# Kernel optimization log

Hardware: AMD Instinct MI355X
Metric: run time of the kernel (lower is better)

Reference implementation:

```python
import jax, jax.numpy as jnp
import numpy as np

UNITS = 64
NUM_LEVELS = 4
ORDER = 4  # order=-1 defaults to num_levels
NUM_FEATURES = 64  # 63 input features + 1 time channel
LEN_TENSORS = NUM_LEVELS * (NUM_LEVELS + 1) // 2  # 10


def setup_inputs() -> dict:
    key = jax.random.key(0)
    k1, k2 = jax.random.split(key)
    X = jax.random.normal(k1, (32, 2048, 63), dtype=jnp.float32)
    # learned low-rank kernel [num_features, len_tensors, units]; small scale keeps
    # higher-level signature products numerically tame
    kernel = jax.random.normal(k2, (NUM_FEATURES, LEN_TENSORS, UNITS), dtype=jnp.float32) * 0.02
    return {"X": X, "kernel": kernel}


def _ecumsum(x):
    # exclusive cumulative sum along time axis (axis=1), forward direction
    return jnp.cumsum(x, axis=1) - x


def reference(X, kernel):
    B, T, _ = X.shape
    # add_time=True: linear time channel in [-1, 1]
    t = jnp.arange(T, dtype=X.dtype) * (2.0 / (T - 1.0)) - 1.0
    time = jnp.broadcast_to(t[None, :, None], (B, T, 1))
    Xa = jnp.concatenate([time, X], axis=-1)  # [B, T, F]
    # low-rank projection: [B, T, len_tensors, units]
    M = jnp.einsum('btf,fku->btku', Xa, kernel)
    # difference=True: forward increments, zero-padded at t=0
    M = jnp.concatenate([jnp.zeros_like(M[:, :1]), M[:, 1:] - M[:, :-1]], axis=1)

    # level 1
    out = jnp.sum(M[..., 0, :], axis=1)  # [B, units]

    k = 1
    for m in range(1, NUM_LEVELS):
        R = [M[..., k, :]]  # list of [B, T, units]
        k += 1
        for i in range(1, m + 1):
            d = min(i + 1, ORDER)
            A = sum(R)
            Mk = M[..., k, :]
            R_next = [Mk * _ecumsum(A)]
            for j in range(1, d):
                R_next.append(Mk * R[j - 1] / jnp.asarray(j + 1, dtype=X.dtype))
            k += 1
            R = R_next
        out = out + jnp.sum(sum(R), axis=1)
    return out
```

## Files before the change

kernel.cpp:

```cpp
#include <hip/hip_runtime.h>


#define TT 2048
#define NFX 63
#define KT 10
#define NU 64
#define NQ 17
#define NCC 32
#define NSEG 4

#define MAPS_BYTES (32u * NCC * NQ * NU * 4u)
#define KWB_BYTES  (2u * 40960u * 2u)
#define PLANE      40960u

typedef __attribute__((ext_vector_type(16))) float f32x16v;
typedef __attribute__((ext_vector_type(8)))  short bf16x8v;

enum {Qo=0, Qa1, Qa3, QaA, Qa6, QaP, QaQ, Qd1, Qd3, QdA, Qd6, QdP, QdQ,
      QtA3, QtP6, QtQP, QtQ6};

__device__ __forceinline__ unsigned short bf16_rne(float x) {
  unsigned int u = __float_as_uint(x);
  unsigned int r = (u + 0x7FFFu + ((u >> 16) & 1u)) >> 16;
  return (unsigned short)r;
}
__device__ __forceinline__ float bf16f(unsigned short h) {
  return __uint_as_float(((unsigned int)h) << 16);
}

__device__ __forceinline__ void compose_maps(const float* q1, const float* q2,
                                             float* r)
{
  r[Qo]  = q1[Qo] + q2[Qo]
         + q2[Qa1]*q1[Qd1] + q2[Qa3]*q1[Qd3] + q2[QaA]*q1[QdA]
         + q2[Qa6]*q1[Qd6] + q2[QaP]*q1[QdP] + q2[QaQ]*q1[QdQ];
  r[Qa1] = q1[Qa1] + q2[Qa1];
  r[Qa3] = q1[Qa3] + q2[Qa3] + q1[QtA3]*q2[QaA];
  r[QaA] = q1[QaA] + q2[QaA];
  r[Qa6] = q1[Qa6] + q2[Qa6] + q1[QtP6]*q2[QaP] + q1[QtQ6]*q2[QaQ];
  r[QaP] = q1[QaP] + q2[QaP] + q1[QtQP]*q2[QaQ];
  r[QaQ] = q1[QaQ] + q2[QaQ];
  r[Qd1] = q1[Qd1] + q2[Qd1];
  r[Qd3] = q1[Qd3] + q2[Qd3];
  r[QdA] = q1[QdA] + q2[QdA] + q2[QtA3]*q1[Qd3];
  r[Qd6] = q1[Qd6] + q2[Qd6];
  r[QdP] = q1[QdP] + q2[QdP] + q2[QtP6]*q1[Qd6];
  r[QdQ] = q1[QdQ] + q2[QdQ] + q2[QtQP]*q1[QdP] + q2[QtQ6]*q1[Qd6];
  r[QtA3] = q1[QtA3] + q2[QtA3];
  r[QtP6] = q1[QtP6] + q2[QtP6];
  r[QtQP] = q1[QtQP] + q2[QtQP];
  r[QtQ6] = q1[QtQ6] + q2[QtQ6] + q2[QtQP]*q1[QtP6];
}

__global__ __launch_bounds__(256)
void lrsig_prep_kernel(const float* __restrict__ Kw,
                       unsigned short* __restrict__ kwb)
{
  int e = blockIdx.x * 256 + threadIdx.x;
  int j  = e & 7;
  int l  = (e >> 3) & 63;
  int ks = (e >> 9) & 3;
  int ub = (e >> 11) & 1;
  int nt = e >> 12;
  int f = ks * 16 + (l >> 5) * 8 + j;
  int u = ub * 32 + (l & 31);
  float x = Kw[(f * KT + nt) * NU + u];
  unsigned short hi = bf16_rne(x);
  unsigned short lo = bf16_rne(x - bf16f(hi));
  kwb[e] = hi;
  kwb[PLANE + e] = lo;
}

template<int KBASE, int NNT>
__device__ __forceinline__ void mfma_phase_pf(
    const unsigned short* __restrict__ kwb,
    const bf16x8v (&ah)[4], const bf16x8v (&al)[4],
    int l, int ub, f32x16v (&acc)[NNT])
{
#pragma unroll
  for (int t = 0; t < NNT; ++t)
#pragma unroll
    for (int i = 0; i < 16; ++i) acc[t][i] = 0.f;

  bf16x8v bh[2][4], bl[2][4];
#pragma unroll
  for (int ks = 0; ks < 4; ++ks) {
    const unsigned short* bp =
        kwb + (((KBASE * 2 + ub) * 4 + ks) * 512) + l * 8;
    bh[0][ks] = *(const bf16x8v*)(bp);
    bl[0][ks] = *(const bf16x8v*)(bp + PLANE);
  }
#pragma unroll
  for (int t = 0; t < NNT; ++t) {
    if (t + 1 < NNT) {
#pragma unroll
      for (int ks = 0; ks < 4; ++ks) {
        const unsigned short* bp =
            kwb + ((((KBASE + t + 1) * 2 + ub) * 4 + ks) * 512) + l * 8;
        bh[(t + 1) & 1][ks] = *(const bf16x8v*)(bp);
        bl[(t + 1) & 1][ks] = *(const bf16x8v*)(bp + PLANE);
      }
    }
#pragma unroll
    for (int ks = 0; ks < 4; ++ks) {
      acc[t] = __builtin_amdgcn_mfma_f32_32x32x16_bf16(ah[ks], bh[t & 1][ks], acc[t], 0, 0, 0);
      acc[t] = __builtin_amdgcn_mfma_f32_32x32x16_bf16(al[ks], bh[t & 1][ks], acc[t], 0, 0, 0);
      acc[t] = __builtin_amdgcn_mfma_f32_32x32x16_bf16(ah[ks], bl[t & 1][ks], acc[t], 0, 0, 0);
    }
  }
}

__global__ __launch_bounds__(256)
void lrsig_chunk_kernel(const float* __restrict__ X,
                        const unsigned short* __restrict__ kwb,
                        float* __restrict__ wmaps)
{
  __shared__ __align__(16) float smemf[8192];
  char* smem = (char*)smemf;
  float* rawf = smemf + 4096;

  const int b   = blockIdx.y;
  const int c   = blockIdx.x;
  const int tid = threadIdx.x;
  const int l   = tid & 63;
  const int w   = tid >> 6;
  const int rt  = w >> 1;
  const int ub  = w & 1;
  const int col = l & 31;
  const int hi8 = l >> 5;
  const int t0  = c * 64;

  float sv[16];
  {
    const float* Xb = X + (size_t)b * TT * NFX;
    const int base = (t0 - 1) * NFX;
#pragma unroll
    for (int ii = 0; ii < 16; ++ii) {
      int i = tid + ii * 256;
      int off = base + i + ((c == 0 && i < NFX) ? NFX : 0);
      sv[ii] = (i < 65 * NFX) ? Xb[off] : 0.f;
    }
  }

  bf16x8v bhA[3][4], blA[3][4];
#pragma unroll
  for (int t = 0; t < 3; ++t)
#pragma unroll
    for (int ks = 0; ks < 4; ++ks) {
      const unsigned short* bp = kwb + (((t * 2 + ub) * 4 + ks) * 512) + l * 8;
      bhA[t][ks] = *(const bf16x8v*)(bp);
      blA[t][ks] = *(const bf16x8v*)(bp + PLANE);
    }

#pragma unroll
  for (int ii = 0; ii < 16; ++ii) {
    int i = tid + ii * 256;
    if (i < 65 * NFX) rawf[i] = sv[ii];
  }
  __syncthreads();

  {
    float v0[16], v1[16];
#pragma unroll
    for (int ii = 0; ii < 16; ++ii) {
      int e = tid + ii * 256;
      if (e < 64 * NFX) { v0[ii] = rawf[e]; v1[ii] = rawf[e + NFX]; }
    }
#pragma unroll
    for (int ii = 0; ii < 16; ++ii) {
      int e = tid + ii * 256;
      if (e < 64 * NFX) {
        int r2 = e / NFX;
        int c2 = e - r2 * NFX;
        float d = v1[ii] - v0[ii];
        unsigned short h  = bf16_rne(d);
        unsigned short lo = bf16_rne(d - bf16f(h));
        int byte = r2 * 128 + ((2 * (c2 + 1)) ^ ((r2 & 7) << 4));
        *(unsigned short*)(smem + byte)        = h;
        *(unsigned short*)(smem + 8192 + byte) = lo;
      }
    }
  }
  if (tid < 64) {
    int r2 = tid;
    float d = (t0 + r2 == 0) ? 0.f : (2.0f / 2047.0f);
    unsigned short h  = bf16_rne(d);
    unsigned short lo = bf16_rne(d - bf16f(h));
    int byte = r2 * 128 + ((0) ^ ((r2 & 7) << 4));
    *(unsigned short*)(smem + byte)        = h;
    *(unsigned short*)(smem + 8192 + byte) = lo;
  }
  __syncthreads();

  const int row = rt * 32 + col;
  const int colbase = ub * 32 + col;

  bf16x8v ah[4], al[4];
#pragma unroll
  for (int ks = 0; ks < 4; ++ks) {
    const int f0 = ks * 16 + hi8 * 8;
    const int abyte = row * 128 + ((2 * f0) ^ ((row & 7) << 4));
    ah[ks] = *(const bf16x8v*)(smem + abyte);
    al[ks] = *(const bf16x8v*)(smem + 8192 + abyte);
  }

  float Ao[4], Aa1[4], Ad1[4];
  {
    f32x16v acc[3];
#pragma unroll
    for (int t = 0; t < 3; ++t)
#pragma unroll
      for (int i = 0; i < 16; ++i) acc[t][i] = 0.f;
#pragma unroll
    for (int ks = 0; ks < 4; ++ks)
#pragma unroll
      for (int t = 0; t < 3; ++t) {
        acc[t] = __builtin_amdgcn_mfma_f32_32x32x16_bf16(ah[ks], bhA[t][ks], acc[t], 0, 0, 0);
        acc[t] = __builtin_amdgcn_mfma_f32_32x32x16_bf16(al[ks], bhA[t][ks], acc[t], 0, 0, 0);
        acc[t] = __builtin_amdgcn_mfma_f32_32x32x16_bf16(ah[ks], blA[t][ks], acc[t], 0, 0, 0);
      }
#pragma unroll
    for (int j = 0; j < 4; ++j) {
      float o = 0.f, a1 = 0.f, lc1 = 0.f;
#pragma unroll
      for (int i = 0; i < 4; ++i) {
        const int r = 4 * j + i;
        float m0 = acc[0][r], m1 = acc[1][r], m2 = acc[2][r];
        o   += m0 + m2 * (lc1 + 0.5f * m1);
        a1  += m2;
        lc1 += m1;
      }
      Ao[j] = o; Aa1[j] = a1; Ad1[j] = lc1;
    }
  }

  float Ba3[4], BaA[4], Bd3[4], BdA[4], BtA3[4];
  {
    f32x16v acc[3];
    mfma_phase_pf<3, 3>(kwb, ah, al, l, ub, acc);
#pragma unroll
    for (int j = 0; j < 4; ++j) {
      float o = 0.f, a3 = 0.f, aA = 0.f, lc3 = 0.f, lcA = 0.f, g4 = 0.f;
#pragma unroll
      for (int i = 0; i < 4; ++i) {
        const int r = 4 * j + i;
        float m3 = acc[0][r], m4 = acc[1][r], m5 = acc[2][r];
        float s0 = m4 * lc3;
        float s1 = 0.5f * m4 * m3;
        o   += m5 * (lcA + 0.5f * s0 + (1.f/3.f) * s1);
        a3  += m5 * (g4 + 0.5f * m4);
        aA  += m5;
        lcA += s0 + s1;
        g4  += m4;
        lc3 += m3;
      }
      Ao[j] += o;
      Ba3[j] = a3; BaA[j] = aA; Bd3[j] = lc3; BdA[j] = lcA; BtA3[j] = g4;
    }
  }

  float tot[NQ];
  {
    f32x16v acc[4];
    mfma_phase_pf<6, 4>(kwb, ah, al, l, ub, acc);
#pragma unroll
    for (int j = 0; j < 4; ++j) {
      float o = 0.f, a6 = 0.f, aP = 0.f, aQ = 0.f;
      float lc6 = 0.f, lcP = 0.f, lcQ = 0.f, g7 = 0.f, g8 = 0.f, hh = 0.f;
#pragma unroll
      for (int i = 0; i < 4; ++i) {
        const int r = 4 * j + i;
        float m6 = acc[0][r], m7 = acc[1][r], m8 = acc[2][r], m9 = acc[3][r];
        float p0 = m7 * lc6;
        float p1 = 0.5f * m7 * m6;
        float q0 = m8 * lcP;
        float q1 = 0.5f * m8 * p0;
        float q2 = (1.f/3.f) * m8 * p1;
        o   += m9 * (lcQ + 0.5f * q0 + (1.f/3.f) * q1 + 0.25f * q2);
        a6  += m9 * (hh + m8 * (0.5f * g7 + (1.f/6.f) * m7));
        aP  += m9 * (g8 + 0.5f * m8);
        aQ  += m9;
        hh  += m8 * (g7 + 0.5f * m7);
        lcP += p0 + p1;
        lcQ += q0 + q1 + q2;
        g7 += m7; g8 += m8; lc6 += m6;
      }
      float mj[NQ];
      mj[Qo] = Ao[j] + o;
      mj[Qa1] = Aa1[j]; mj[Qa3] = Ba3[j]; mj[QaA] = BaA[j];
      mj[Qa6] = a6;     mj[QaP] = aP;     mj[QaQ] = aQ;
      mj[Qd1] = Ad1[j]; mj[Qd3] = Bd3[j]; mj[QdA] = BdA[j];
      mj[Qd6] = lc6;    mj[QdP] = lcP;    mj[QdQ] = lcQ;
      mj[QtA3] = BtA3[j]; mj[QtP6] = g7;  mj[QtQP] = g8; mj[QtQ6] = hh;

      float q1v[NQ], q2v[NQ], m8r[NQ];
#pragma unroll
      for (int q = 0; q < NQ; ++q) {
        float oth = __shfl_xor(mj[q], 32);
        q1v[q] = hi8 ? oth : mj[q];
        q2v[q] = hi8 ? mj[q] : oth;
      }
      compose_maps(q1v, q2v, m8r);

      if (j == 0) {
#pragma unroll
        for (int q = 0; q < NQ; ++q) tot[q] = m8r[q];
      } else {
        float nt_[NQ];
        compose_maps(tot, m8r, nt_);
#pragma unroll
        for (int q = 0; q < NQ; ++q) tot[q] = nt_[q];
      }
    }
  }

  if (hi8 == 0) {
    float* p = &rawf[(rt * NQ) * NU + colbase];
#pragma unroll
    for (int q = 0; q < NQ; ++q) p[q * NU] = tot[q];
  }
  __syncthreads();

  if (tid < NU) {
    const int uu = tid;
    float q1v[NQ], q2v[NQ], rv[NQ];
#pragma unroll
    for (int q = 0; q < NQ; ++q) {
      q1v[q] = rawf[(0 * NQ + q) * NU + uu];
      q2v[q] = rawf[(1 * NQ + q) * NU + uu];
    }
    compose_maps(q1v, q2v, rv);
    float* p = &wmaps[(((size_t)b * NCC + c) * NQ) * NU + uu];
#pragma unroll
    for (int q = 0; q < NQ; ++q) p[q * NU] = rv[q];
  }
}

__global__ __launch_bounds__(256)
void lrsig_partial_kernel(const float* __restrict__ wmaps,
                          float* __restrict__ part)
{
  const int b   = blockIdx.x;
  const int seg = threadIdx.x >> 6;
  const int u   = threadIdx.x & 63;
  float tot[NQ];
  {
    const float* p0 = &wmaps[(((size_t)b * NCC + seg * 8) * NQ) * NU + u];
#pragma unroll
    for (int q = 0; q < NQ; ++q) tot[q] = p0[q * NU];
  }
  for (int i = 1; i < 8; ++i) {
    const float* p = &wmaps[(((size_t)b * NCC + seg * 8 + i) * NQ) * NU + u];
    float m[NQ], r[NQ];
#pragma unroll
    for (int q = 0; q < NQ; ++q) m[q] = p[q * NU];
    compose_maps(tot, m, r);
#pragma unroll
    for (int q = 0; q < NQ; ++q) tot[q] = r[q];
  }
  float* d = &part[(((size_t)b * NSEG + seg) * NQ) * NU + u];
#pragma unroll
  for (int q = 0; q < NQ; ++q) d[q * NU] = tot[q];
}

__global__ __launch_bounds__(64)
void lrsig_final_kernel(const float* __restrict__ part,
                        float* __restrict__ out)
{
  const int b = blockIdx.x;
  const int u = threadIdx.x;
  float c1 = 0.f, c3 = 0.f, cA = 0.f, c6 = 0.f, cP = 0.f, cQ = 0.f, o = 0.f;
#pragma unroll
  for (int s = 0; s < NSEG; ++s) {
    const float* p = &part[(((size_t)b * NSEG + s) * NQ) * NU + u];
    float q[NQ];
#pragma unroll
    for (int i = 0; i < NQ; ++i) q[i] = p[i * NU];
    o  += q[0] + q[1]*c1 + q[2]*c3 + q[3]*cA + q[4]*c6 + q[5]*cP + q[6]*cQ;
    cA += q[13]*c3 + q[9];
    cQ += q[15]*cP + q[16]*c6 + q[12];
    cP += q[14]*c6 + q[11];
    c1 += q[7]; c3 += q[8]; c6 += q[10];
  }
  out[b * 64 + u] = o;
}

extern "C" void kernel_launch(void* const* d_in, const int* in_sizes, int n_in,
                              void* d_out, int out_size, void* d_ws, size_t ws_size,
                              hipStream_t stream) {
  const float* X  = (const float*)d_in[0];
  const float* Kw = (const float*)d_in[1];
  float* out = (float*)d_out;
  float* wmaps = (float*)d_ws;
  unsigned short* kwb = (unsigned short*)((char*)d_ws + MAPS_BYTES);
  float* part = (float*)((char*)d_ws + MAPS_BYTES + KWB_BYTES);

  hipLaunchKernelGGL(lrsig_prep_kernel, dim3(160), dim3(256), 0, stream,
                     Kw, kwb);
  hipLaunchKernelGGL(lrsig_chunk_kernel, dim3(NCC, 32), dim3(256), 0, stream,
                     X, kwb, wmaps);
  hipLaunchKernelGGL(lrsig_partial_kernel, dim3(32), dim3(256), 0, stream,
                     wmaps, part);
  hipLaunchKernelGGL(lrsig_final_kernel, dim3(32), dim3(64), 0, stream,
                     part, out);
}
```

Before: 48.35 us.

## Fuse partial and final combine kernels, stream B operands, tree-reduce chunk maps

Merges the partial and final combine kernels into one launch that passes the per-segment maps through shared memory instead of a global scratch buffer. This removes one kernel launch and a global round trip. In the chunk kernel, the B operands for all ten projection tiles are now streamed through one double buffer, replacing the register-resident phase-A preload and the templated helper. The sequential fold of the four 8-row maps becomes a balanced tree of compositions, which shortens the dependency chain but keeps more values live in registers.

After: 48.60 us. No clear change (+0.5%).

```diff
diff --git a/kernel.cpp b/kernel.cpp
--- a/kernel.cpp
+++ b/kernel.cpp
@@ -10,7 +10,6 @@
 #define NSEG 4
 
 #define MAPS_BYTES (32u * NCC * NQ * NU * 4u)
-#define KWB_BYTES  (2u * 40960u * 2u)
 #define PLANE      40960u
 
 typedef __attribute__((ext_vector_type(16))) float f32x16v;
@@ -71,44 +70,24 @@
   kwb[PLANE + e] = lo;
 }
 
-template<int KBASE, int NNT>
-__device__ __forceinline__ void mfma_phase_pf(
-    const unsigned short* __restrict__ kwb,
-    const bf16x8v (&ah)[4], const bf16x8v (&al)[4],
-    int l, int ub, f32x16v (&acc)[NNT])
-{
-#pragma unroll
-  for (int t = 0; t < NNT; ++t)
-#pragma unroll
-    for (int i = 0; i < 16; ++i) acc[t][i] = 0.f;
-
-  bf16x8v bh[2][4], bl[2][4];
-#pragma unroll
-  for (int ks = 0; ks < 4; ++ks) {
-    const unsigned short* bp =
-        kwb + (((KBASE * 2 + ub) * 4 + ks) * 512) + l * 8;
-    bh[0][ks] = *(const bf16x8v*)(bp);
-    bl[0][ks] = *(const bf16x8v*)(bp + PLANE);
-  }
-#pragma unroll
-  for (int t = 0; t < NNT; ++t) {
-    if (t + 1 < NNT) {
-#pragma unroll
-      for (int ks = 0; ks < 4; ++ks) {
-        const unsigned short* bp =
-            kwb + ((((KBASE + t + 1) * 2 + ub) * 4 + ks) * 512) + l * 8;
-        bh[(t + 1) & 1][ks] = *(const bf16x8v*)(bp);
-        bl[(t + 1) & 1][ks] = *(const bf16x8v*)(bp + PLANE);
-      }
-    }
-#pragma unroll
-    for (int ks = 0; ks < 4; ++ks) {
-      acc[t] = __builtin_amdgcn_mfma_f32_32x32x16_bf16(ah[ks], bh[t & 1][ks], acc[t], 0, 0, 0);
-      acc[t] = __builtin_amdgcn_mfma_f32_32x32x16_bf16(al[ks], bh[t & 1][ks], acc[t], 0, 0, 0);
-      acc[t] = __builtin_amdgcn_mfma_f32_32x32x16_bf16(ah[ks], bl[t & 1][ks], acc[t], 0, 0, 0);
-    }
-  }
-}
+#define LOADB(BUF, S) do {                                                   \
+  _Pragma("unroll")                                                          \
+  for (int ks = 0; ks < 4; ++ks) {                                           \
+    const unsigned short* bp = kwb + ((((S) * 2 + ub) * 4 + ks) * 512) + l*8;\
+    bh##BUF[ks] = *(const bf16x8v*)(bp);                                     \
+    bl##BUF[ks] = *(const bf16x8v*)(bp + PLANE);                             \
+  } } while (0)
+
+#define MFMA12(ACC, BUF) do {                                                \
+  _Pragma("unroll")                                                          \
+  for (int ks = 0; ks < 4; ++ks) {                                           \
+    ACC = __builtin_amdgcn_mfma_f32_32x32x16_bf16(ah[ks], bh##BUF[ks], ACC, 0,0,0); \
+    ACC = __builtin_amdgcn_mfma_f32_32x32x16_bf16(al[ks], bh##BUF[ks], ACC, 0,0,0); \
+    ACC = __builtin_amdgcn_mfma_f32_32x32x16_bf16(ah[ks], bl##BUF[ks], ACC, 0,0,0); \
+  } } while (0)
+
+#define ZERO(ACC) do { _Pragma("unroll")                                     \
+  for (int zi = 0; zi < 16; ++zi) ACC[zi] = 0.f; } while (0)
 
 __global__ __launch_bounds__(256)
 void lrsig_chunk_kernel(const float* __restrict__ X,
@@ -142,15 +121,8 @@
     }
   }
 
-  bf16x8v bhA[3][4], blA[3][4];
-#pragma unroll
-  for (int t = 0; t < 3; ++t)
-#pragma unroll
-    for (int ks = 0; ks < 4; ++ks) {
-      const unsigned short* bp = kwb + (((t * 2 + ub) * 4 + ks) * 512) + l * 8;
-      bhA[t][ks] = *(const bf16x8v*)(bp);
-      blA[t][ks] = *(const bf16x8v*)(bp + PLANE);
-    }
+  bf16x8v bh0[4], bl0[4], bh1[4], bl1[4];
+  LOADB(0, 0);
 
 #pragma unroll
   for (int ii = 0; ii < 16; ++ii) {
@@ -205,27 +177,21 @@
   }
 
   float Ao[4], Aa1[4], Ad1[4];
-  {
-    f32x16v acc[3];
-#pragma unroll
-    for (int t = 0; t < 3; ++t)
-#pragma unroll
-      for (int i = 0; i < 16; ++i) acc[t][i] = 0.f;
-#pragma unroll
-    for (int ks = 0; ks < 4; ++ks)
-#pragma unroll
-      for (int t = 0; t < 3; ++t) {
-        acc[t] = __builtin_amdgcn_mfma_f32_32x32x16_bf16(ah[ks], bhA[t][ks], acc[t], 0, 0, 0);
-        acc[t] = __builtin_amdgcn_mfma_f32_32x32x16_bf16(al[ks], bhA[t][ks], acc[t], 0, 0, 0);
-        acc[t] = __builtin_amdgcn_mfma_f32_32x32x16_bf16(ah[ks], blA[t][ks], acc[t], 0, 0, 0);
-      }
+  float Ba3[4], BaA[4], Bd3[4], BdA[4], BtA3[4];
+
+  {
+    f32x16v accA[3];
+    ZERO(accA[0]); ZERO(accA[1]); ZERO(accA[2]);
+    LOADB(1, 1);  MFMA12(accA[0], 0);
+    LOADB(0, 2);  MFMA12(accA[1], 1);
+    LOADB(1, 3);  MFMA12(accA[2], 0);
 #pragma unroll
     for (int j = 0; j < 4; ++j) {
       float o = 0.f, a1 = 0.f, lc1 = 0.f;
 #pragma unroll
       for (int i = 0; i < 4; ++i) {
         const int r = 4 * j + i;
-        float m0 = acc[0][r], m1 = acc[1][r], m2 = acc[2][r];
+        float m0 = accA[0][r], m1 = accA[1][r], m2 = accA[2][r];
         o   += m0 + m2 * (lc1 + 0.5f * m1);
         a1  += m2;
         lc1 += m1;
@@ -234,17 +200,19 @@
     }
   }
 
-  float Ba3[4], BaA[4], Bd3[4], BdA[4], BtA3[4];
-  {
-    f32x16v acc[3];
-    mfma_phase_pf<3, 3>(kwb, ah, al, l, ub, acc);
+  {
+    f32x16v accB[3];
+    ZERO(accB[0]); ZERO(accB[1]); ZERO(accB[2]);
+    LOADB(0, 4);  MFMA12(accB[0], 1);
+    LOADB(1, 5);  MFMA12(accB[1], 0);
+    LOADB(0, 6);  MFMA12(accB[2], 1);
 #pragma unroll
     for (int j = 0; j < 4; ++j) {
       float o = 0.f, a3 = 0.f, aA = 0.f, lc3 = 0.f, lcA = 0.f, g4 = 0.f;
 #pragma unroll
       for (int i = 0; i < 4; ++i) {
         const int r = 4 * j + i;
-        float m3 = acc[0][r], m4 = acc[1][r], m5 = acc[2][r];
+        float m3 = accB[0][r], m4 = accB[1][r], m5 = accB[2][r];
         float s0 = m4 * lc3;
         float s1 = 0.5f * m4 * m3;
         o   += m5 * (lcA + 0.5f * s0 + (1.f/3.f) * s1);
@@ -261,8 +229,14 @@
 
   float tot[NQ];
   {
-    f32x16v acc[4];
-    mfma_phase_pf<6, 4>(kwb, ah, al, l, ub, acc);
+    f32x16v accC[4];
+    ZERO(accC[0]); ZERO(accC[1]); ZERO(accC[2]); ZERO(accC[3]);
+    LOADB(1, 7);  MFMA12(accC[0], 0);
+    LOADB(0, 8);  MFMA12(accC[1], 1);
+    LOADB(1, 9);  MFMA12(accC[2], 0);
+                  MFMA12(accC[3], 1);
+
+    float mjv[4][NQ];
 #pragma unroll
     for (int j = 0; j < 4; ++j) {
       float o = 0.f, a6 = 0.f, aP = 0.f, aQ = 0.f;
@@ -270,7 +244,7 @@
 #pragma unroll
       for (int i = 0; i < 4; ++i) {
         const int r = 4 * j + i;
-        float m6 = acc[0][r], m7 = acc[1][r], m8 = acc[2][r], m9 = acc[3][r];
+        float m6 = accC[0][r], m7 = accC[1][r], m8 = accC[2][r], m9 = accC[3][r];
         float p0 = m7 * lc6;
         float p1 = 0.5f * m7 * m6;
         float q0 = m8 * lcP;
@@ -285,33 +259,31 @@
         lcQ += q0 + q1 + q2;
         g7 += m7; g8 += m8; lc6 += m6;
       }
-      float mj[NQ];
-      mj[Qo] = Ao[j] + o;
-      mj[Qa1] = Aa1[j]; mj[Qa3] = Ba3[j]; mj[QaA] = BaA[j];
-      mj[Qa6] = a6;     mj[QaP] = aP;     mj[QaQ] = aQ;
-      mj[Qd1] = Ad1[j]; mj[Qd3] = Bd3[j]; mj[QdA] = BdA[j];
-      mj[Qd6] = lc6;    mj[QdP] = lcP;    mj[QdQ] = lcQ;
-      mj[QtA3] = BtA3[j]; mj[QtP6] = g7;  mj[QtQP] = g8; mj[QtQ6] = hh;
-
-      float q1v[NQ], q2v[NQ], m8r[NQ];
+      mjv[j][Qo] = Ao[j] + o;
+      mjv[j][Qa1] = Aa1[j]; mjv[j][Qa3] = Ba3[j]; mjv[j][QaA] = BaA[j];
+      mjv[j][Qa6] = a6;     mjv[j][QaP] = aP;     mjv[j][QaQ] = aQ;
+      mjv[j][Qd1] = Ad1[j]; mjv[j][Qd3] = Bd3[j]; mjv[j][QdA] = BdA[j];
+      mjv[j][Qd6] = lc6;    mjv[j][QdP] = lcP;    mjv[j][QdQ] = lcQ;
+      mjv[j][QtA3] = BtA3[j]; mjv[j][QtP6] = g7;
+      mjv[j][QtQP] = g8;      mjv[j][QtQ6] = hh;
+    }
+
+    float m8v[4][NQ];
+#pragma unroll
+    for (int j = 0; j < 4; ++j) {
+      float q1v[NQ], q2v[NQ];
 #pragma unroll
       for (int q = 0; q < NQ; ++q) {
-        float oth = __shfl_xor(mj[q], 32);
-        q1v[q] = hi8 ? oth : mj[q];
-        q2v[q] = hi8 ? mj[q] : oth;
-      }
-      compose_maps(q1v, q2v, m8r);
-
-      if (j == 0) {
-#pragma unroll
-        for (int q = 0; q < NQ; ++q) tot[q] = m8r[q];
-      } else {
-        float nt_[NQ];
-        compose_maps(tot, m8r, nt_);
-#pragma unroll
-        for (int q = 0; q < NQ; ++q) tot[q] = nt_[q];
-      }
-    }
+        float oth = __shfl_xor(mjv[j][q], 32);
+        q1v[q] = hi8 ? oth : mjv[j][q];
+        q2v[q] = hi8 ? mjv[j][q] : oth;
+      }
+      compose_maps(q1v, q2v, m8v[j]);
+    }
+    float m16a[NQ], m16b[NQ];
+    compose_maps(m8v[0], m8v[1], m16a);
+    compose_maps(m8v[2], m8v[3], m16b);
+    compose_maps(m16a, m16b, tot);
   }
 
   if (hi8 == 0) {
@@ -337,12 +309,14 @@
 }
 
 __global__ __launch_bounds__(256)
-void lrsig_partial_kernel(const float* __restrict__ wmaps,
-                          float* __restrict__ part)
+void lrsig_combine_kernel(const float* __restrict__ wmaps,
+                          float* __restrict__ out)
 {
+  __shared__ float sm[NSEG * NQ * NU];
   const int b   = blockIdx.x;
   const int seg = threadIdx.x >> 6;
   const int u   = threadIdx.x & 63;
+
   float tot[NQ];
   {
     const float* p0 = &wmaps[(((size_t)b * NCC + seg * 8) * NQ) * NU + u];
@@ -358,31 +332,26 @@
 #pragma unroll
     for (int q = 0; q < NQ; ++q) tot[q] = r[q];
   }
-  float* d = &part[(((size_t)b * NSEG + seg) * NQ) * NU + u];
-#pragma unroll
-  for (int q = 0; q < NQ; ++q) d[q * NU] = tot[q];
-}
-
-__global__ __launch_bounds__(64)
-void lrsig_final_kernel(const float* __restrict__ part,
-                        float* __restrict__ out)
-{
-  const int b = blockIdx.x;
-  const int u = threadIdx.x;
-  float c1 = 0.f, c3 = 0.f, cA = 0.f, c6 = 0.f, cP = 0.f, cQ = 0.f, o = 0.f;
-#pragma unroll
-  for (int s = 0; s < NSEG; ++s) {
-    const float* p = &part[(((size_t)b * NSEG + s) * NQ) * NU + u];
-    float q[NQ];
-#pragma unroll
-    for (int i = 0; i < NQ; ++i) q[i] = p[i * NU];
-    o  += q[0] + q[1]*c1 + q[2]*c3 + q[3]*cA + q[4]*c6 + q[5]*cP + q[6]*cQ;
-    cA += q[13]*c3 + q[9];
-    cQ += q[15]*cP + q[16]*c6 + q[12];
-    cP += q[14]*c6 + q[11];
-    c1 += q[7]; c3 += q[8]; c6 += q[10];
-  }
-  out[b * 64 + u] = o;
+#pragma unroll
+  for (int q = 0; q < NQ; ++q) sm[(seg * NQ + q) * NU + u] = tot[q];
+  __syncthreads();
+
+  if (threadIdx.x < NU) {
+    const int uu = threadIdx.x;
+    float c1 = 0.f, c3 = 0.f, cA = 0.f, c6 = 0.f, cP = 0.f, cQ = 0.f, o = 0.f;
+#pragma unroll
+    for (int s = 0; s < NSEG; ++s) {
+      float q[NQ];
+#pragma unroll
+      for (int i = 0; i < NQ; ++i) q[i] = sm[(s * NQ + i) * NU + uu];
+      o  += q[0] + q[1]*c1 + q[2]*c3 + q[3]*cA + q[4]*c6 + q[5]*cP + q[6]*cQ;
+      cA += q[13]*c3 + q[9];
+      cQ += q[15]*cP + q[16]*c6 + q[12];
+      cP += q[14]*c6 + q[11];
+      c1 += q[7]; c3 += q[8]; c6 += q[10];
+    }
+    out[b * 64 + uu] = o;
+  }
 }
 
 extern "C" void kernel_launch(void* const* d_in, const int* in_sizes, int n_in,
@@ -393,14 +362,11 @@
   float* out = (float*)d_out;
   float* wmaps = (float*)d_ws;
   unsigned short* kwb = (unsigned short*)((char*)d_ws + MAPS_BYTES);
-  float* part = (float*)((char*)d_ws + MAPS_BYTES + KWB_BYTES);
 
   hipLaunchKernelGGL(lrsig_prep_kernel, dim3(160), dim3(256), 0, stream,
                      Kw, kwb);
   hipLaunchKernelGGL(lrsig_chunk_kernel, dim3(NCC, 32), dim3(256), 0, stream,
                      X, kwb, wmaps);
-  hipLaunchKernelGGL(lrsig_partial_kernel, dim3(32), dim3(256), 0, stream,
-                     wmaps, part);
-  hipLaunchKernelGGL(lrsig_final_kernel, dim3(32), dim3(64), 0, stream,
-                     part, out);
-}
+  hipLaunchKernelGGL(lrsig_combine_kernel, dim3(32), dim3(256), 0, stream,
+                     wmaps, out);
+}
```
